# Optimization experiments

Hardware: AMD Instinct MI355X
Metric: run time of the kernel (lower is better)

Reference implementation:

```python
import jax, jax.numpy as jnp
import numpy as np

AUDIO_DIM = 256
VIDEO_DIM = 256
CONV_CH = 128
FUSED_DIM = 512
EPS = 1e-12


def _interp_linear(x, t_out):
    # x: [B, T_in, D]; torch F.interpolate(mode='linear', align_corners=False)
    t_in = x.shape[1]
    scale = t_in / t_out
    src = (jnp.arange(t_out, dtype=jnp.float32) + 0.5) * scale - 0.5
    src = jnp.maximum(src, 0.0)
    i0 = jnp.floor(src).astype(jnp.int32)
    i0 = jnp.minimum(i0, t_in - 1)
    i1 = jnp.minimum(i0 + 1, t_in - 1)
    w = (src - i0.astype(jnp.float32))[None, :, None]
    return x[:, i0, :] * (1.0 - w) + x[:, i1, :] * w


def _conv1d(x, w, b, pad):
    # x: [B, C, T], w: [O, I, K]
    y = jax.lax.conv_general_dilated(x, w, window_strides=(1,), padding=[(pad, pad)],
                                     dimension_numbers=('NCH', 'OIH', 'NCH'))
    return y + b[None, :, None]


def setup_inputs() -> dict:
    key = jax.random.key(0)
    ks = jax.random.split(key, 12)
    B, Ta, Tv = 16, 2048, 1024

    def xavier(k, shape):
        fan_out, fan_in = shape[0], int(np.prod(shape[1:]))
        std = float(np.sqrt(2.0 / (fan_in + fan_out)))
        return jax.random.normal(k, shape, dtype=jnp.float32) * std

    return {
        'audio_features': jax.random.normal(ks[0], (B, Ta, AUDIO_DIM), dtype=jnp.float32),
        'video_features': jax.random.normal(ks[1], (B, Tv, VIDEO_DIM), dtype=jnp.float32),
        'a3_w': xavier(ks[2], (CONV_CH, AUDIO_DIM, 3)), 'a3_b': jnp.zeros((CONV_CH,), jnp.float32),
        'a5_w': xavier(ks[3], (CONV_CH, AUDIO_DIM, 5)), 'a5_b': jnp.zeros((CONV_CH,), jnp.float32),
        'v3_w': xavier(ks[4], (CONV_CH, VIDEO_DIM, 3)), 'v3_b': jnp.zeros((CONV_CH,), jnp.float32),
        'v5_w': xavier(ks[5], (CONV_CH, VIDEO_DIM, 5)), 'v5_b': jnp.zeros((CONV_CH,), jnp.float32),
        'proj_w': xavier(ks[6], (FUSED_DIM, FUSED_DIM)), 'proj_b': jnp.zeros((FUSED_DIM,), jnp.float32),
    }


def reference(audio_features, video_features, a3_w, a3_b, a5_w, a5_b,
              v3_w, v3_b, v5_w, v5_b, proj_w, proj_b):
    Ta, Tv = audio_features.shape[1], video_features.shape[1]
    T = max((Ta + Tv) // 2, 1)
    # temporal alignment to common length T
    a = _interp_linear(audio_features, T)  # [B, T, 256]
    v = _interp_linear(video_features, T)  # [B, T, 256]

    gelu = lambda x: jax.nn.gelu(x, approximate=False)
    a_in = jnp.swapaxes(a, 1, 2)  # [B, 256, T]
    v_in = jnp.swapaxes(v, 1, 2)
    a_multi = jnp.concatenate([gelu(_conv1d(a_in, a3_w, a3_b, 1)),
                               gelu(_conv1d(a_in, a5_w, a5_b, 2))], axis=1)  # [B, 256, T]
    v_multi = jnp.concatenate([gelu(_conv1d(v_in, v3_w, v3_b, 1)),
                               gelu(_conv1d(v_in, v5_w, v5_b, 2))], axis=1)
    a_multi = jnp.swapaxes(a_multi, 1, 2)  # [B, T, 256]
    v_multi = jnp.swapaxes(v_multi, 1, 2)

    # cosine-similarity cross attention (torch F.normalize eps=1e-12)
    a_norm = a_multi / jnp.maximum(jnp.linalg.norm(a_multi, axis=-1, keepdims=True), EPS)
    v_norm = v_multi / jnp.maximum(jnp.linalg.norm(v_multi, axis=-1, keepdims=True), EPS)
    sim = jnp.einsum('btd,bsd->bts', a_norm, v_norm)  # [B, T, T]

    attn_a2v = jax.nn.softmax(sim, axis=-1)              # audio attends video
    attn_v2a = jnp.swapaxes(jax.nn.softmax(sim, axis=1), 1, 2)  # video attends audio
    a_enh = jnp.einsum('bts,bsd->btd', attn_a2v, v_multi)
    v_enh = jnp.einsum('bst,btd->bsd', jnp.swapaxes(attn_v2a, 1, 2), a_multi)
    # (equivalently v_enh = attn_v2a @ a_multi)
    v_enh = jnp.einsum('bts,bsd->btd', attn_v2a, a_multi)

    fused = jnp.concatenate([a + a_enh, v + v_enh], axis=-1)  # [B, T, 512]
    out = gelu(fused @ proj_w.T + proj_b)
    # dropout is identity in eval mode
    return out
```

## Files before the change

kernel.cpp:

```cpp
#include <hip/hip_runtime.h>
#include <math.h>

#define BATCH 16
#define TA 2048
#define TV 1024
#define TT 1536
#define DIM 256
#define FD 512

typedef unsigned short u16;
typedef unsigned int u32;
typedef short bf16x8 __attribute__((ext_vector_type(8)));
typedef float f32x4 __attribute__((ext_vector_type(4)));

__device__ __forceinline__ float bf2f(u16 u) {
  union { u32 i; float f; } v; v.i = ((u32)u) << 16; return v.f;
}
__device__ __forceinline__ u16 f2bf(float f) {
  union { float f; u32 i; } v; v.f = f;
  return (u16)((v.i + 0x7fffu + ((v.i >> 16) & 1u)) >> 16);
}
__device__ __forceinline__ float gelu_f(float x) {
  return 0.5f * x * (1.0f + erff(x * 0.70710678118654752440f));
}
__device__ __forceinline__ void async16(const u16* g, u16* l) {
  __builtin_amdgcn_global_load_lds((const __attribute__((address_space(1))) void*)g,
                                   (__attribute__((address_space(3))) void*)l, 16, 0, 0);
}

__global__ __launch_bounds__(256) void k_prep(
    const float* __restrict__ a3w, const float* __restrict__ a5w,
    const float* __restrict__ v3w, const float* __restrict__ v5w,
    const float* __restrict__ pw,
    u16* __restrict__ w3a, u16* __restrict__ w5a,
    u16* __restrict__ w3v, u16* __restrict__ w5v, u16* __restrict__ wp) {
  int idx = blockIdx.x * 256 + threadIdx.x;
  if (idx < 524288) {
    int e, ktaps;
    const float* src;
    u16* dst;
    if (idx < 98304)       { e = idx;          ktaps = 3; src = a3w; dst = w3a; }
    else if (idx < 262144) { e = idx - 98304;  ktaps = 5; src = a5w; dst = w5a; }
    else if (idx < 360448) { e = idx - 262144; ktaps = 3; src = v3w; dst = w3v; }
    else                   { e = idx - 360448; ktaps = 5; src = v5w; dst = w5v; }
    int kk = e >> 12, r = e & 4095;
    int j = r & 7, unit = r >> 3;
    int fb = unit >> 6, rem = unit & 63;
    int q = rem >> 4, colp = rem & 15;
    int o = fb * 16 + colp;
    int tap = kk >> 3;
    int c = (kk & 7) * 32 + q * 8 + j;
    dst[e] = f2bf(src[(o * 256 + c) * ktaps + tap]);
  } else if (idx < 786432) {
    int t = idx - 524288;
    wp[t] = f2bf(pw[t]);
  }
}

__global__ __launch_bounds__(256) void k_interp(const float* __restrict__ in,
                                                u16* __restrict__ out,
                                                int t_in, float scale) {
  int b = blockIdx.y;
  int i = blockIdx.x * 256 + threadIdx.x;
  int t = i >> 5, dg = i & 31;
  float src = ((float)t + 0.5f) * scale - 0.5f;
  src = fmaxf(src, 0.0f);
  int i0 = (int)floorf(src);
  if (i0 > t_in - 1) i0 = t_in - 1;
  int i1 = i0 + 1; if (i1 > t_in - 1) i1 = t_in - 1;
  float w = src - (float)i0;
  float om = 1.0f - w;
  const float4* p0 = (const float4*)(in + ((size_t)(b * t_in + i0)) * DIM + dg * 8);
  const float4* p1 = (const float4*)(in + ((size_t)(b * t_in + i1)) * DIM + dg * 8);
  float4 x0a = p0[0], x0b = p0[1], x1a = p1[0], x1b = p1[1];
  u16 r[8];
  r[0] = f2bf(x0a.x * om + x1a.x * w); r[1] = f2bf(x0a.y * om + x1a.y * w);
  r[2] = f2bf(x0a.z * om + x1a.z * w); r[3] = f2bf(x0a.w * om + x1a.w * w);
  r[4] = f2bf(x0b.x * om + x1b.x * w); r[5] = f2bf(x0b.y * om + x1b.y * w);
  r[6] = f2bf(x0b.z * om + x1b.z * w); r[7] = f2bf(x0b.w * om + x1b.w * w);
  u32 w0 = (u32)r[0] | ((u32)r[1] << 16), w1 = (u32)r[2] | ((u32)r[3] << 16);
  u32 w2 = (u32)r[4] | ((u32)r[5] << 16), w3 = (u32)r[6] | ((u32)r[7] << 16);
  *(uint4*)(out + ((size_t)(b * TT + t)) * DIM + dg * 8) = make_uint4(w0, w1, w2, w3);
}

__global__ __launch_bounds__(256) void k_zero(float* __restrict__ p, int n) {
  int i = blockIdx.x * 256 + threadIdx.x;
  if (i < n) p[i] = 0.f;
}

template <int TAPS>
__global__ __launch_bounds__(256) void k_convN(
    const u16* __restrict__ xa, const u16* __restrict__ xv,
    const u16* __restrict__ Wa, const u16* __restrict__ Wv,
    const float* __restrict__ ba, const float* __restrict__ bv,
    u16* __restrict__ outMa, u16* __restrict__ outMv,
    u16* __restrict__ outTa, u16* __restrict__ outTv,
    float* __restrict__ nsqa, float* __restrict__ nsqv) {
  constexpr int S = TAPS * 8;
  constexpr int OFF = (TAPS == 3) ? 1 : 2;
  constexpr int CHB = (TAPS == 3) ? 0 : 128;
  __shared__ __align__(16) u16 xs[68 * 264];
  __shared__ __align__(16) u16 Bs[2 * 4096];
  u16* tb = xs;
  int b = blockIdx.y, t0 = blockIdx.x * 64;
  int isv = blockIdx.z;
  const u16* xin = isv ? xv : xa;
  const u16* W   = isv ? Wv : Wa;
  const float* bias = isv ? bv : ba;
  u16* outM  = isv ? outMv : outMa;
  u16* outT  = isv ? outTv : outTa;
  float* nsq = isv ? nsqv : nsqa;
  int tid = threadIdx.x, wave = tid >> 6, lane = tid & 63;
  int col = lane & 15, quad = lane >> 4;

  for (int i = tid; i < 68 * 32; i += 256) {
    int row = i >> 5, un = i & 31;
    int t = t0 + row - 2;
    uint4 val = make_uint4(0, 0, 0, 0);
    if (t >= 0 && t < TT) val = *(const uint4*)(xin + ((size_t)(b * TT + t)) * DIM + un * 8);
    *(uint4*)(xs + row * 264 + un * 8) = val;
  }
  const u16* Wb = W + wave * 1024 + lane * 8;
  u16* BsW = Bs + wave * 1024;
  async16(Wb, BsW);
  async16(Wb + 512, BsW + 512);

  f32x4 acc[4][2];
  f32x4 zz = {0.f, 0.f, 0.f, 0.f};
#pragma unroll
  for (int rt = 0; rt < 4; rt++) { acc[rt][0] = zz; acc[rt][1] = zz; }

  const u16* afp = xs + (col + 2) * 264 + quad * 8;
  const u16* bfp = Bs + wave * 1024 + quad * 128 + col * 8;

#pragma unroll
  for (int s = 0; s < S; s++) {
    __syncthreads();
    if (s + 1 < S) {
      const u16* src = Wb + (size_t)(s + 1) * 4096;
      u16* dst = Bs + ((s + 1) & 1) * 4096 + wave * 1024;
      async16(src, dst);
      async16(src + 512, dst + 512);
    }
    int shift = (s >> 3) - OFF;
    int c0 = (s & 7) * 32;
    bf16x8 af[4];
#pragma unroll
    for (int rt = 0; rt < 4; rt++)
      af[rt] = *(const bf16x8*)(afp + (rt * 16 + shift) * 264 + c0);
    bf16x8 bf0 = *(const bf16x8*)(bfp + (s & 1) * 4096);
    bf16x8 bf1 = *(const bf16x8*)(bfp + (s & 1) * 4096 + 512);
#pragma unroll
    for (int rt = 0; rt < 4; rt++) {
      acc[rt][0] = __builtin_amdgcn_mfma_f32_16x16x32_bf16(af[rt], bf0, acc[rt][0], 0, 0, 0);
      acc[rt][1] = __builtin_amdgcn_mfma_f32_16x16x32_bf16(af[rt], bf1, acc[rt][1], 0, 0, 0);
    }
  }
  __syncthreads();

  float bia0 = bias[wave * 32 + col];
  float bia1 = bias[wave * 32 + 16 + col];
  float ss[4][4];
#pragma unroll
  for (int rt = 0; rt < 4; rt++)
#pragma unroll
    for (int r = 0; r < 4; r++) ss[rt][r] = 0.f;
#pragma unroll
  for (int rt = 0; rt < 4; rt++)
#pragma unroll
    for (int h = 0; h < 2; h++) {
      float bia = h ? bia1 : bia0;
      int chL = wave * 32 + h * 16 + col;
#pragma unroll
      for (int r = 0; r < 4; r++) {
        float g = gelu_f(acc[rt][h][r] + bia);
        ss[rt][r] += g * g;
        int trow = rt * 16 + quad * 4 + r;
        u16 gb = f2bf(g);
        tb[chL * 72 + trow] = gb;
        outM[((size_t)(b * TT + t0 + trow)) * DIM + CHB + chL] = gb;
      }
    }
#pragma unroll
  for (int rt = 0; rt < 4; rt++)
#pragma unroll
    for (int r = 0; r < 4; r++) {
      float v = ss[rt][r];
      v += __shfl_xor(v, 1, 64); v += __shfl_xor(v, 2, 64);
      v += __shfl_xor(v, 4, 64); v += __shfl_xor(v, 8, 64);
      if (col == 0)
        atomicAdd(&nsq[b * TT + t0 + rt * 16 + quad * 4 + r], v);
    }
  __syncthreads();
  {
    int ch = tid >> 1, half = tid & 1;
    uint4* dst = (uint4*)(outT + ((size_t)(b * 256 + CHB + ch)) * TT + t0 + half * 32);
#pragma unroll
    for (int i = 0; i < 4; i++)
      dst[i] = *(const uint4*)(tb + ch * 72 + half * 32 + i * 8);
  }
}

__global__ __launch_bounds__(256, 2) void k_flash(
    const u16* __restrict__ aM, const u16* __restrict__ vM,
    const u16* __restrict__ aMT, const u16* __restrict__ vMT,
    const float* __restrict__ naq, const float* __restrict__ nvq,
    const u16* __restrict__ a_itp, const u16* __restrict__ v_itp,
    u16* __restrict__ fused) {
  __shared__ __align__(16) u16 sKV[8 * 64 * 32];
  __shared__ __align__(16) u16 sKT[2 * 256 * 32];
  __shared__ __align__(16) u16 sE[2 * 32 * 64];
  __shared__ float sDen[2][64];

  int wgid = blockIdx.x;
  int xcd = wgid & 7, j = wgid >> 3;
  int g = xcd + 8 * (j / 24);
  int m0 = (j % 24) * 64;
  int b = g & 15, z = g >> 4;
  const u16* Q    = z ? vM : aM;
  const u16* KV   = z ? aM : vM;
  const u16* KVT  = z ? aMT : vMT;
  const float* nq = z ? nvq : naq;
  const float* nk = z ? naq : nvq;
  const u16* itp  = z ? v_itp : a_itp;
  int dstoff = z ? 256 : 0;

  int tid = threadIdx.x, w = tid >> 6, lane = tid & 63;
  int mg = w >> 1, ng = w & 1;
  int col = lane & 15, quad = lane >> 4;
  int li = lane >> 2;
  int sq = (lane & 3) ^ ((lane >> 3) & 3);

  const u16* KVb = KV + ((size_t)b * TT) * DIM;
  const u16* KTb = KVT + ((size_t)b * 256) * TT;
  const float* nkB = nk + (size_t)b * TT;

  auto stageKV = [&](int n0s) {
#pragma unroll
    for (int kk = 0; kk < 2; kk++) {
      int kt = w * 2 + kk;
#pragma unroll
      for (int i = 0; i < 4; i++)
        async16(KVb + (size_t)(n0s + i * 16 + li) * DIM + kt * 32 + sq * 8,
                sKV + kt * 2048 + i * 512);
    }
  };
  auto stageKT = [&](int n0s) {
#pragma unroll
    for (int kn = 0; kn < 2; kn++)
#pragma unroll
      for (int i = 0; i < 4; i++)
        async16(KTb + (size_t)(w * 64 + i * 16 + li) * TT + n0s + kn * 32 + sq * 8,
                sKT + kn * 8192 + w * 2048 + i * 512);
  };

  bf16x8 qf[2][8];
  const u16* Qb = Q + ((size_t)(b * TT + m0 + mg * 32)) * DIM;
#pragma unroll
  for (int mt = 0; mt < 2; mt++)
#pragma unroll
    for (int kt = 0; kt < 8; kt++)
      qf[mt][kt] = *(const bf16x8*)(Qb + (size_t)(mt * 16 + col) * DIM + kt * 32 + quad * 8);

  float sra[2][4];
#pragma unroll
  for (int mt = 0; mt < 2; mt++)
#pragma unroll
    for (int r = 0; r < 4; r++)
      sra[mt][r] = 1.0f / fmaxf(
          sqrtf(nq[(size_t)b * TT + m0 + mg * 32 + mt * 16 + quad * 4 + r]), 1e-12f);

  int c0 = ng * 32 + col, c1 = ng * 32 + 16 + col;
  float rvRaw0 = nkB[c0], rvRaw1 = nkB[c1];

  f32x4 acc[2][8];
  f32x4 zz = {0.f, 0.f, 0.f, 0.f};
#pragma unroll
  for (int mt = 0; mt < 2; mt++)
#pragma unroll
    for (int dt = 0; dt < 8; dt++) acc[mt][dt] = zz;
  float den[2][4];
#pragma unroll
  for (int mt = 0; mt < 2; mt++)
#pragma unroll
    for (int r = 0; r < 4; r++) den[mt][r] = 0.f;

  stageKV(0);
  stageKT(0);
  __syncthreads();

  for (int t = 0; t < 24; t++) {
    int n0 = t * 64;
    f32x4 sc[2][2];
    sc[0][0] = zz; sc[0][1] = zz; sc[1][0] = zz; sc[1][1] = zz;
#pragma unroll
    for (int kt = 0; kt < 8; kt++)
#pragma unroll
      for (int nt = 0; nt < 2; nt++) {
        int row = ng * 32 + nt * 16 + col;
        bf16x8 bf = *(const bf16x8*)(sKV + kt * 2048 + row * 32 +
                                     ((quad ^ ((row >> 1) & 3)) << 3));
        sc[0][nt] = __builtin_amdgcn_mfma_f32_16x16x32_bf16(qf[0][kt], bf, sc[0][nt], 0, 0, 0);
        sc[1][nt] = __builtin_amdgcn_mfma_f32_16x16x32_bf16(qf[1][kt], bf, sc[1][nt], 0, 0, 0);
      }
    float rvi[2];
    rvi[0] = 1.0f / fmaxf(sqrtf(rvRaw0), 1e-12f);
    rvi[1] = 1.0f / fmaxf(sqrtf(rvRaw1), 1e-12f);
#pragma unroll
    for (int mt = 0; mt < 2; mt++)
#pragma unroll
      for (int nt = 0; nt < 2; nt++) {
        int c = ng * 32 + nt * 16 + col;
        float rv = rvi[nt];
#pragma unroll
        for (int r = 0; r < 4; r++) {
          float e = __expf(sc[mt][nt][r] * sra[mt][r] * rv);
          den[mt][r] += e;
          int row = mt * 16 + quad * 4 + r;
          sE[mg * 2048 + row * 64 + (((c >> 3) ^ ((row >> 1) & 7)) << 3) + (c & 7)] =
              f2bf(e);
        }
      }

    __builtin_amdgcn_sched_barrier(0);
    asm volatile("s_waitcnt vmcnt(0) lgkmcnt(0)" ::: "memory");
    __builtin_amdgcn_s_barrier();
    __builtin_amdgcn_sched_barrier(0);

    int nn = (t < 23) ? (n0 + 64) : 0;
    float rvA = nkB[nn + c0], rvB = nkB[nn + c1];
    if (t < 23) stageKV(n0 + 64);
#pragma unroll
    for (int kn = 0; kn < 2; kn++) {
      bf16x8 ea0, ea1;
      {
        int row = col;
        ea0 = *(const bf16x8*)(sE + mg * 2048 + row * 64 +
                               (((kn * 4 + quad) ^ ((row >> 1) & 7)) << 3));
        row = 16 + col;
        ea1 = *(const bf16x8*)(sE + mg * 2048 + row * 64 +
                               (((kn * 4 + quad) ^ ((row >> 1) & 7)) << 3));
      }
#pragma unroll
      for (int dt = 0; dt < 8; dt++) {
        int drow = ng * 128 + dt * 16 + col;
        bf16x8 bf = *(const bf16x8*)(sKT + kn * 8192 + drow * 32 +
                                     ((quad ^ ((drow >> 1) & 3)) << 3));
        acc[0][dt] = __builtin_amdgcn_mfma_f32_16x16x32_bf16(ea0, bf, acc[0][dt], 0, 0, 0);
        acc[1][dt] = __builtin_amdgcn_mfma_f32_16x16x32_bf16(ea1, bf, acc[1][dt], 0, 0, 0);
      }
    }

    __builtin_amdgcn_sched_barrier(0);
    asm volatile("s_waitcnt lgkmcnt(0)" ::: "memory");
    __builtin_amdgcn_s_barrier();
    __builtin_amdgcn_sched_barrier(0);

    if (t < 23) stageKT(n0 + 64);
    __builtin_amdgcn_sched_barrier(0);
    asm volatile("s_waitcnt vmcnt(8) lgkmcnt(0)" ::: "memory");
    __builtin_amdgcn_s_barrier();
    __builtin_amdgcn_sched_barrier(0);

    rvRaw0 = rvA; rvRaw1 = rvB;
  }

#pragma unroll
  for (int mt = 0; mt < 2; mt++)
#pragma unroll
    for (int r = 0; r < 4; r++) {
      float v = den[mt][r];
      v += __shfl_xor(v, 1, 64); v += __shfl_xor(v, 2, 64);
      v += __shfl_xor(v, 4, 64); v += __shfl_xor(v, 8, 64);
      if (col == 0) sDen[ng][mg * 32 + mt * 16 + quad * 4 + r] = v;
    }
  __syncthreads();

#pragma unroll
  for (int mt = 0; mt < 2; mt++)
#pragma unroll
    for (int r = 0; r < 4; r++) {
      int row = mg * 32 + mt * 16 + quad * 4 + r;
      int t = m0 + row;
      float dinv = 1.0f / (sDen[0][row] + sDen[1][row]);
      const u16* ip = itp + ((size_t)(b * TT + t)) * DIM;
      u16* op = fused + ((size_t)(b * TT + t)) * FD + dstoff;
#pragma unroll
      for (int dt = 0; dt < 8; dt++) {
        int d = ng * 128 + dt * 16 + col;
        float val = acc[mt][dt][r] * dinv + bf2f(ip[d]);
        op[d] = f2bf(val);
      }
    }
}

__global__ __launch_bounds__(256) void k_proj(const u16* __restrict__ Am,
                                              const u16* __restrict__ Bw,
                                              const float* __restrict__ bias,
                                              float* __restrict__ out) {
  __shared__ u16 As[128 * 32], Bs[128 * 32];
  int m0 = blockIdx.y * 128, n0 = blockIdx.x * 128;
  int tid = threadIdx.x, wave = tid >> 6, lane = tid & 63;
  int col = lane & 15, quad = lane >> 4;
  int wm = (wave >> 1) * 64, wn = (wave & 1) * 64;
  int lrow = lane >> 2, lcol = (lane & 3) * 8;
  const u16* Ab = Am + (size_t)m0 * FD;
  const u16* Bb = Bw + (size_t)n0 * FD;
  f32x4 acc[4][4];
  f32x4 zz = {0.f, 0.f, 0.f, 0.f};
#pragma unroll
  for (int i = 0; i < 4; i++)
#pragma unroll
    for (int j = 0; j < 4; j++) acc[i][j] = zz;

  for (int kt = 0; kt < 16; kt++) {
    int k0 = kt * 32;
    __syncthreads();
#pragma unroll
    for (int i = 0; i < 2; i++) {
      int rb = wave * 32 + i * 16;
      async16(Ab + ((size_t)(rb + lrow)) * FD + k0 + lcol, As + rb * 32);
      async16(Bb + ((size_t)(rb + lrow)) * FD + k0 + lcol, Bs + rb * 32);
    }
    __syncthreads();
    bf16x8 af[4], bfr[4];
#pragma unroll
    for (int mt = 0; mt < 4; mt++) af[mt] = *(const bf16x8*)(As + (wm + mt * 16 + col) * 32 + quad * 8);
#pragma unroll
    for (int nt = 0; nt < 4; nt++) bfr[nt] = *(const bf16x8*)(Bs + (wn + nt * 16 + col) * 32 + quad * 8);
#pragma unroll
    for (int mt = 0; mt < 4; mt++)
#pragma unroll
      for (int nt = 0; nt < 4; nt++)
        acc[mt][nt] = __builtin_amdgcn_mfma_f32_16x16x32_bf16(af[mt], bfr[nt], acc[mt][nt], 0, 0, 0);
  }
#pragma unroll
  for (int nt = 0; nt < 4; nt++) {
    float bia = bias[n0 + wn + nt * 16 + col];
#pragma unroll
    for (int mt = 0; mt < 4; mt++)
#pragma unroll
      for (int r = 0; r < 4; r++) {
        int row = m0 + wm + mt * 16 + quad * 4 + r;
        int cc = n0 + wn + nt * 16 + col;
        out[(size_t)row * FD + cc] = gelu_f(acc[mt][nt][r] + bia);
      }
  }
}

extern "C" void kernel_launch(void* const* d_in, const int* in_sizes, int n_in,
                              void* d_out, int out_size, void* d_ws, size_t ws_size,
                              hipStream_t stream) {
  const float* audio = (const float*)d_in[0];
  const float* video = (const float*)d_in[1];
  const float* a3w = (const float*)d_in[2];
  const float* a3b = (const float*)d_in[3];
  const float* a5w = (const float*)d_in[4];
  const float* a5b = (const float*)d_in[5];
  const float* v3w = (const float*)d_in[6];
  const float* v3b = (const float*)d_in[7];
  const float* v5w = (const float*)d_in[8];
  const float* v5b = (const float*)d_in[9];
  const float* pw  = (const float*)d_in[10];
  const float* pb  = (const float*)d_in[11];
  float* out = (float*)d_out;

  char* ws = (char*)d_ws;
  size_t off = 0;
  auto alloc = [&](size_t bytes) {
    char* p = ws + off;
    off += (bytes + 255) & ~(size_t)255;
    return p;
  };
  size_t szItp = (size_t)BATCH * TT * DIM * 2;
  u16* a_itp = (u16*)alloc(szItp);
  u16* v_itp = (u16*)alloc(szItp);
  u16* aM  = (u16*)alloc(szItp);
  u16* vM  = (u16*)alloc(szItp);
  u16* aMT = (u16*)alloc(szItp);
  u16* vMT = (u16*)alloc(szItp);
  float* naq = (float*)alloc((size_t)BATCH * TT * 4);
  float* nvq = (float*)alloc((size_t)BATCH * TT * 4);
  u16* fusedb = (u16*)alloc((size_t)BATCH * TT * FD * 2);
  u16* w3a = (u16*)alloc(3 * 128 * 256 * 2);
  u16* w5a = (u16*)alloc(5 * 128 * 256 * 2);
  u16* w3v = (u16*)alloc(3 * 128 * 256 * 2);
  u16* w5v = (u16*)alloc(5 * 128 * 256 * 2);
  u16* wp  = (u16*)alloc(512 * 512 * 2);

  k_prep<<<3072, 256, 0, stream>>>(a3w, a5w, v3w, v5w, pw, w3a, w5a, w3v, w5v, wp);
  k_interp<<<dim3(192, 16), 256, 0, stream>>>(audio, a_itp, TA, (float)((double)TA / TT));
  k_interp<<<dim3(192, 16), 256, 0, stream>>>(video, v_itp, TV, (float)((double)TV / TT));
  k_zero<<<192, 256, 0, stream>>>(naq, 2 * BATCH * TT);
  k_convN<3><<<dim3(24, 16, 2), 256, 0, stream>>>(a_itp, v_itp, w3a, w3v, a3b, v3b,
                                                  aM, vM, aMT, vMT, naq, nvq);
  k_convN<5><<<dim3(24, 16, 2), 256, 0, stream>>>(a_itp, v_itp, w5a, w5v, a5b, v5b,
                                                  aM, vM, aMT, vMT, naq, nvq);
  k_flash<<<768, 256, 0, stream>>>(aM, vM, aMT, vMT, naq, nvq, a_itp, v_itp, fusedb);
  k_proj<<<dim3(4, 192), 256, 0, stream>>>(fusedb, wp, pb, out);
}
```

Before: 336.7 us.

## Transpose flash score MFMA, pack bf16 stores, double-buffer projection, fold zeroing

The flash kernel now computes the score tile transposed (swapped MFMA operands), so each lane holds four consecutive key columns. This allows vectorized norm loads, packed bf16 conversion via v_cvt_pk_bf16_f32 with 8-byte LDS stores, and a cheaper denominator reduction across two shuffles. s_setprio is raised around the MFMA phases. The projection GEMM gets double-buffered LDS with one barrier per k-step, and the norm-accumulator zeroing moves into the prep kernel, removing one launch. The risks are the new swizzle slot math for sE and the single barrier per iteration in k_proj, which must still order reuse of each buffer.

After: 349.7 us. 3.9% more time.

```diff
diff --git a/kernel.cpp b/kernel.cpp
--- a/kernel.cpp
+++ b/kernel.cpp
@@ -20,6 +20,11 @@
   union { float f; u32 i; } v; v.f = f;
   return (u16)((v.i + 0x7fffu + ((v.i >> 16) & 1u)) >> 16);
 }
+__device__ __forceinline__ u32 cvtpk_bf16(float a, float b) {
+  u32 r;
+  asm("v_cvt_pk_bf16_f32 %0, %1, %2" : "=v"(r) : "v"(a), "v"(b));
+  return r;
+}
 __device__ __forceinline__ float gelu_f(float x) {
   return 0.5f * x * (1.0f + erff(x * 0.70710678118654752440f));
 }
@@ -33,7 +38,8 @@
     const float* __restrict__ v3w, const float* __restrict__ v5w,
     const float* __restrict__ pw,
     u16* __restrict__ w3a, u16* __restrict__ w5a,
-    u16* __restrict__ w3v, u16* __restrict__ w5v, u16* __restrict__ wp) {
+    u16* __restrict__ w3v, u16* __restrict__ w5v, u16* __restrict__ wp,
+    float* __restrict__ nz) {
   int idx = blockIdx.x * 256 + threadIdx.x;
   if (idx < 524288) {
     int e, ktaps;
@@ -54,6 +60,8 @@
   } else if (idx < 786432) {
     int t = idx - 524288;
     wp[t] = f2bf(pw[t]);
+  } else if (idx < 835584) {
+    nz[idx - 786432] = 0.f;
   }
 }
 
@@ -83,11 +91,6 @@
   *(uint4*)(out + ((size_t)(b * TT + t)) * DIM + dg * 8) = make_uint4(w0, w1, w2, w3);
 }
 
-__global__ __launch_bounds__(256) void k_zero(float* __restrict__ p, int n) {
-  int i = blockIdx.x * 256 + threadIdx.x;
-  if (i < n) p[i] = 0.f;
-}
-
 template <int TAPS>
 __global__ __launch_bounds__(256) void k_convN(
     const u16* __restrict__ xa, const u16* __restrict__ xv,
@@ -262,16 +265,15 @@
     for (int kt = 0; kt < 8; kt++)
       qf[mt][kt] = *(const bf16x8*)(Qb + (size_t)(mt * 16 + col) * DIM + kt * 32 + quad * 8);
 
-  float sra[2][4];
+  float sraC[2];
 #pragma unroll
   for (int mt = 0; mt < 2; mt++)
-#pragma unroll
-    for (int r = 0; r < 4; r++)
-      sra[mt][r] = 1.0f / fmaxf(
-          sqrtf(nq[(size_t)b * TT + m0 + mg * 32 + mt * 16 + quad * 4 + r]), 1e-12f);
-
-  int c0 = ng * 32 + col, c1 = ng * 32 + 16 + col;
-  float rvRaw0 = nkB[c0], rvRaw1 = nkB[c1];
+    sraC[mt] = 1.0f / fmaxf(
+        sqrtf(nq[(size_t)b * TT + m0 + mg * 32 + mt * 16 + col]), 1e-12f);
+
+  f32x4 rvc[2], rvn[2];
+  rvc[0] = *(const f32x4*)(nkB + ng * 32 + 4 * quad);
+  rvc[1] = *(const f32x4*)(nkB + ng * 32 + 16 + 4 * quad);
 
   f32x4 acc[2][8];
   f32x4 zz = {0.f, 0.f, 0.f, 0.f};
@@ -279,11 +281,8 @@
   for (int mt = 0; mt < 2; mt++)
 #pragma unroll
     for (int dt = 0; dt < 8; dt++) acc[mt][dt] = zz;
-  float den[2][4];
-#pragma unroll
-  for (int mt = 0; mt < 2; mt++)
-#pragma unroll
-    for (int r = 0; r < 4; r++) den[mt][r] = 0.f;
+  float den[2];
+  den[0] = 0.f; den[1] = 0.f;
 
   stageKV(0);
   stageKT(0);
@@ -291,8 +290,9 @@
 
   for (int t = 0; t < 24; t++) {
     int n0 = t * 64;
-    f32x4 sc[2][2];
-    sc[0][0] = zz; sc[0][1] = zz; sc[1][0] = zz; sc[1][1] = zz;
+    f32x4 scT[2][2];
+    scT[0][0] = zz; scT[0][1] = zz; scT[1][0] = zz; scT[1][1] = zz;
+    __builtin_amdgcn_s_setprio(1);
 #pragma unroll
     for (int kt = 0; kt < 8; kt++)
 #pragma unroll
@@ -300,36 +300,47 @@
         int row = ng * 32 + nt * 16 + col;
         bf16x8 bf = *(const bf16x8*)(sKV + kt * 2048 + row * 32 +
                                      ((quad ^ ((row >> 1) & 3)) << 3));
-        sc[0][nt] = __builtin_amdgcn_mfma_f32_16x16x32_bf16(qf[0][kt], bf, sc[0][nt], 0, 0, 0);
-        sc[1][nt] = __builtin_amdgcn_mfma_f32_16x16x32_bf16(qf[1][kt], bf, sc[1][nt], 0, 0, 0);
-      }
-    float rvi[2];
-    rvi[0] = 1.0f / fmaxf(sqrtf(rvRaw0), 1e-12f);
-    rvi[1] = 1.0f / fmaxf(sqrtf(rvRaw1), 1e-12f);
-#pragma unroll
-    for (int mt = 0; mt < 2; mt++)
+        scT[0][nt] = __builtin_amdgcn_mfma_f32_16x16x32_bf16(bf, qf[0][kt], scT[0][nt], 0, 0, 0);
+        scT[1][nt] = __builtin_amdgcn_mfma_f32_16x16x32_bf16(bf, qf[1][kt], scT[1][nt], 0, 0, 0);
+      }
+    __builtin_amdgcn_s_setprio(0);
+
+    f32x4 ri[2];
+#pragma unroll
+    for (int nt = 0; nt < 2; nt++)
+#pragma unroll
+      for (int r = 0; r < 4; r++)
+        ri[nt][r] = 1.0f / fmaxf(sqrtf(rvc[nt][r]), 1e-12f);
+#pragma unroll
+    for (int mt = 0; mt < 2; mt++) {
+      float sm = sraC[mt];
+      int row = mt * 16 + col;
+      int rx = (row >> 1) & 7;
 #pragma unroll
       for (int nt = 0; nt < 2; nt++) {
-        int c = ng * 32 + nt * 16 + col;
-        float rv = rvi[nt];
-#pragma unroll
-        for (int r = 0; r < 4; r++) {
-          float e = __expf(sc[mt][nt][r] * sra[mt][r] * rv);
-          den[mt][r] += e;
-          int row = mt * 16 + quad * 4 + r;
-          sE[mg * 2048 + row * 64 + (((c >> 3) ^ ((row >> 1) & 7)) << 3) + (c & 7)] =
-              f2bf(e);
-        }
-      }
+        float e0 = __expf(scT[mt][nt][0] * sm * ri[nt][0]);
+        float e1 = __expf(scT[mt][nt][1] * sm * ri[nt][1]);
+        float e2 = __expf(scT[mt][nt][2] * sm * ri[nt][2]);
+        float e3 = __expf(scT[mt][nt][3] * sm * ri[nt][3]);
+        den[mt] += (e0 + e1) + (e2 + e3);
+        u32 p01 = cvtpk_bf16(e0, e1), p23 = cvtpk_bf16(e2, e3);
+        int slot = (4 * ng + 2 * nt + (quad >> 1)) ^ rx;
+        *(uint2*)(sE + mg * 2048 + row * 64 + slot * 8 + 4 * (quad & 1)) =
+            make_uint2(p01, p23);
+      }
+    }
 
     __builtin_amdgcn_sched_barrier(0);
     asm volatile("s_waitcnt vmcnt(0) lgkmcnt(0)" ::: "memory");
     __builtin_amdgcn_s_barrier();
     __builtin_amdgcn_sched_barrier(0);
 
-    int nn = (t < 23) ? (n0 + 64) : 0;
-    float rvA = nkB[nn + c0], rvB = nkB[nn + c1];
-    if (t < 23) stageKV(n0 + 64);
+    if (t < 23) {
+      rvn[0] = *(const f32x4*)(nkB + n0 + 64 + ng * 32 + 4 * quad);
+      rvn[1] = *(const f32x4*)(nkB + n0 + 64 + ng * 32 + 16 + 4 * quad);
+      stageKV(n0 + 64);
+    }
+    __builtin_amdgcn_s_setprio(1);
 #pragma unroll
     for (int kn = 0; kn < 2; kn++) {
       bf16x8 ea0, ea1;
@@ -350,6 +361,7 @@
         acc[1][dt] = __builtin_amdgcn_mfma_f32_16x16x32_bf16(ea1, bf, acc[1][dt], 0, 0, 0);
       }
     }
+    __builtin_amdgcn_s_setprio(0);
 
     __builtin_amdgcn_sched_barrier(0);
     asm volatile("s_waitcnt lgkmcnt(0)" ::: "memory");
@@ -362,18 +374,16 @@
     __builtin_amdgcn_s_barrier();
     __builtin_amdgcn_sched_barrier(0);
 
-    rvRaw0 = rvA; rvRaw1 = rvB;
-  }
-
-#pragma unroll
-  for (int mt = 0; mt < 2; mt++)
-#pragma unroll
-    for (int r = 0; r < 4; r++) {
-      float v = den[mt][r];
-      v += __shfl_xor(v, 1, 64); v += __shfl_xor(v, 2, 64);
-      v += __shfl_xor(v, 4, 64); v += __shfl_xor(v, 8, 64);
-      if (col == 0) sDen[ng][mg * 32 + mt * 16 + quad * 4 + r] = v;
-    }
+    rvc[0] = rvn[0]; rvc[1] = rvn[1];
+  }
+
+#pragma unroll
+  for (int mt = 0; mt < 2; mt++) {
+    float v = den[mt];
+    v += __shfl_xor(v, 16, 64);
+    v += __shfl_xor(v, 32, 64);
+    if (quad == 0) sDen[ng][mg * 32 + mt * 16 + col] = v;
+  }
   __syncthreads();
 
 #pragma unroll
@@ -398,7 +408,7 @@
                                               const u16* __restrict__ Bw,
                                               const float* __restrict__ bias,
                                               float* __restrict__ out) {
-  __shared__ u16 As[128 * 32], Bs[128 * 32];
+  __shared__ __align__(16) u16 As[2][128 * 32], Bs[2][128 * 32];
   int m0 = blockIdx.y * 128, n0 = blockIdx.x * 128;
   int tid = threadIdx.x, wave = tid >> 6, lane = tid & 63;
   int col = lane & 15, quad = lane >> 4;
@@ -413,26 +423,32 @@
 #pragma unroll
     for (int j = 0; j < 4; j++) acc[i][j] = zz;
 
-  for (int kt = 0; kt < 16; kt++) {
-    int k0 = kt * 32;
-    __syncthreads();
+  auto stage = [&](int kt) {
+    int bsel = kt & 1, k0 = kt * 32;
 #pragma unroll
     for (int i = 0; i < 2; i++) {
       int rb = wave * 32 + i * 16;
-      async16(Ab + ((size_t)(rb + lrow)) * FD + k0 + lcol, As + rb * 32);
-      async16(Bb + ((size_t)(rb + lrow)) * FD + k0 + lcol, Bs + rb * 32);
-    }
-    __syncthreads();
+      async16(Ab + ((size_t)(rb + lrow)) * FD + k0 + lcol, &As[bsel][rb * 32]);
+      async16(Bb + ((size_t)(rb + lrow)) * FD + k0 + lcol, &Bs[bsel][rb * 32]);
+    }
+  };
+
+  stage(0);
+  __syncthreads();
+  for (int kt = 0; kt < 16; kt++) {
+    if (kt < 15) stage(kt + 1);
+    int bsel = kt & 1;
     bf16x8 af[4], bfr[4];
 #pragma unroll
-    for (int mt = 0; mt < 4; mt++) af[mt] = *(const bf16x8*)(As + (wm + mt * 16 + col) * 32 + quad * 8);
-#pragma unroll
-    for (int nt = 0; nt < 4; nt++) bfr[nt] = *(const bf16x8*)(Bs + (wn + nt * 16 + col) * 32 + quad * 8);
+    for (int mt = 0; mt < 4; mt++) af[mt] = *(const bf16x8*)(&As[bsel][0] + (wm + mt * 16 + col) * 32 + quad * 8);
+#pragma unroll
+    for (int nt = 0; nt < 4; nt++) bfr[nt] = *(const bf16x8*)(&Bs[bsel][0] + (wn + nt * 16 + col) * 32 + quad * 8);
 #pragma unroll
     for (int mt = 0; mt < 4; mt++)
 #pragma unroll
       for (int nt = 0; nt < 4; nt++)
         acc[mt][nt] = __builtin_amdgcn_mfma_f32_16x16x32_bf16(af[mt], bfr[nt], acc[mt][nt], 0, 0, 0);
+    __syncthreads();
   }
 #pragma unroll
   for (int nt = 0; nt < 4; nt++) {
@@ -488,10 +504,9 @@
   u16* w5v = (u16*)alloc(5 * 128 * 256 * 2);
   u16* wp  = (u16*)alloc(512 * 512 * 2);
 
-  k_prep<<<3072, 256, 0, stream>>>(a3w, a5w, v3w, v5w, pw, w3a, w5a, w3v, w5v, wp);
+  k_prep<<<3264, 256, 0, stream>>>(a3w, a5w, v3w, v5w, pw, w3a, w5a, w3v, w5v, wp, naq);
   k_interp<<<dim3(192, 16), 256, 0, stream>>>(audio, a_itp, TA, (float)((double)TA / TT));
   k_interp<<<dim3(192, 16), 256, 0, stream>>>(video, v_itp, TV, (float)((double)TV / TT));
-  k_zero<<<192, 256, 0, stream>>>(naq, 2 * BATCH * TT);
   k_convN<3><<<dim3(24, 16, 2), 256, 0, stream>>>(a_itp, v_itp, w3a, w3v, a3b, v3b,
                                                   aM, vM, aMT, vMT, naq, nvq);
   k_convN<5><<<dim3(24, 16, 2), 256, 0, stream>>>(a_itp, v_itp, w5a, w5v, a5b, v5b,
```
